# Kernel tuning notes

Measured on AMD Instinct MI355X. Metric: run time of the kernel, lower is better.

The kernel has to match this reference:

```python
import jax, jax.numpy as jnp
import numpy as np
from jax import lax


def setup_inputs() -> dict:
    key = jax.random.key(0)
    k1, k2 = jax.random.split(key)
    B, H, W, Cin, Cout, kh, kw = 16, 128, 128, 128, 128, 3, 3
    X = jax.random.normal(k1, (B, H, W, Cin), dtype=jnp.float32)
    kernel = jax.random.normal(k2, (B, kh, kw, Cin, Cout), dtype=jnp.float32) * 0.05
    return {"X": X, "kernel": kernel}


def _conv_one(x, k):
    # x: [H, W, Cin]; k: [kh, kw, Cin, Cout] -> [H', W', Cout]
    out = lax.conv_general_dilated(
        x[None],  # [1, H, W, Cin]
        k,
        window_strides=(1, 1),
        padding='VALID',
        dimension_numbers=('NHWC', 'HWIO', 'NHWC'),
    )
    return out[0]


def reference(X, kernel):
    # Per-sample dynamic-filter conv: each batch element convolved with its own
    # [kh, kw, Cin, Cout] filter. Equivalent to the TF depthwise-reshape trick
    # followed by reduce_sum over the input-channel axis.
    return jax.vmap(_conv_one)(X, kernel)  # [B, H', W', Cout]
```

## Files before the change

### kernel.cpp

```cpp
#include <hip/hip_runtime.h>
#include <cstdint>

#define OWD 126
#define MTOT 15876

typedef short bf16x8 __attribute__((ext_vector_type(8)));
typedef float f32x4  __attribute__((ext_vector_type(4)));

#define BT_ELEMS  (16u * 128u * 1152u)
#define XBF_ELEMS (16u * 128u * 128u * 128u)
#define WS_NEEDED ((size_t)(BT_ELEMS + XBF_ELEMS) * 2)

__device__ __forceinline__ uint16_t f2bf(float f) {
    union { float f; uint32_t u; } v;
    v.f = f;
    uint32_t u = v.u;
    return (uint16_t)((u + 0x7FFFu + ((u >> 16) & 1u)) >> 16);
}

__device__ __forceinline__ uint32_t pk2(float a, float b) {
    return (uint32_t)f2bf(a) | ((uint32_t)f2bf(b) << 16);
}

__device__ __forceinline__ void gl_lds16(const uint16_t* g, uint16_t* l) {
    __builtin_amdgcn_global_load_lds(
        (const __attribute__((address_space(1))) uint32_t*)g,
        (__attribute__((address_space(3))) uint32_t*)l, 16, 0, 0);
}

__global__ __launch_bounds__(256) void kprep(const float* __restrict__ Kin,
                                             uint16_t* __restrict__ Bt) {
    const int rs = blockIdx.x;
    const int b  = blockIdx.y;
    const int t  = threadIdx.x;
    const int n  = t & 127;
    const int og = t >> 7;

    const float* src = Kin + (((size_t)b * 9 + rs) << 14);
    uint16_t*    dst = Bt + ((size_t)b * 128 + n) * 1152 + rs * 128;

#pragma unroll
    for (int o = 0; o < 8; ++o) {
        const int oct = og * 8 + o;
        const float* s0 = src + (oct * 8) * 128 + n;
        uint4 p;
        p.x = pk2(s0[0 * 128], s0[1 * 128]);
        p.y = pk2(s0[2 * 128], s0[3 * 128]);
        p.z = pk2(s0[4 * 128], s0[5 * 128]);
        p.w = pk2(s0[6 * 128], s0[7 * 128]);
        *(uint4*)(dst + oct * 8) = p;
    }
}

__global__ __launch_bounds__(256) void xprep(const float* __restrict__ X,
                                             uint16_t* __restrict__ Xbf) {
    const size_t i = ((size_t)blockIdx.x * 256 + threadIdx.x) * 8;
    const float4 a = *(const float4*)(X + i);
    const float4 b = *(const float4*)(X + i + 4);
    uint4 p;
    p.x = pk2(a.x, a.y);
    p.y = pk2(a.z, a.w);
    p.z = pk2(b.x, b.y);
    p.w = pk2(b.z, b.w);
    *(uint4*)(Xbf + i) = p;
}

__global__ __launch_bounds__(256) void conv_mfma_c(const uint16_t* __restrict__ Xbf,
                                                   const uint16_t* __restrict__ Bt,
                                                   float* __restrict__ Out) {
    __shared__ __align__(16) uint16_t lds[3][256 * 32];

    const int id    = blockIdx.x + 125 * blockIdx.y;
    const int nid   = (id & 7) * 250 + (id >> 3);
    const int mtile = nid % 125;
    const int b     = nid / 125;

    const int tid  = threadIdx.x;
    const int lane = tid & 63;
    const int wave = tid >> 6;
    const int wm   = (wave & 1) << 6;
    const int wn   = (wave >> 1) << 6;
    const int l15  = lane & 15;
    const int quad = lane >> 4;

    const int l2 = lane >> 2;
    const int kc = (lane & 3) ^ ((lane >> 3) & 3);
    const uint16_t* Asrc[2];
    const uint16_t* Bsrc[2];
#pragma unroll
    for (int i = 0; i < 2; ++i) {
        const int row = wave * 32 + i * 16 + l2;
        int m = mtile * 128 + row;
        if (m >= MTOT) m = MTOT - 1;
        const int oh = m / OWD, ow = m - oh * OWD;
        Asrc[i] = Xbf + (((size_t)b * 128 + oh) * 128 + ow) * 128 + kc * 8;
        Bsrc[i] = Bt + ((size_t)b * 128 + row) * 1152 + kc * 8;
    }
    const int dbase = wave * 1024 + lane * 8;

    f32x4 acc[4][4];
#pragma unroll
    for (int i = 0; i < 4; ++i)
#pragma unroll
        for (int j = 0; j < 4; ++j)
            acc[i][j] = (f32x4){0.f, 0.f, 0.f, 0.f};

#define STAGE(t_, bu_)                                                      \
    {                                                                       \
        const int rs_ = (t_) >> 2;                                         \
        const int c0_ = ((t_) & 3) << 5;                                   \
        const int r_  = (rs_ * 11) >> 5;                \
        const int s_  = rs_ - r_ * 3;                                      \
        const int ao_ = (r_ * 128 + s_) * 128 + c0_;                       \
        const int bo_ = rs_ * 128 + c0_;                                   \
        uint16_t* Ad_ = &lds[bu_][dbase];                                  \
        uint16_t* Bd_ = &lds[bu_][4096 + dbase];                           \
        _Pragma("unroll")                                                  \
        for (int i_ = 0; i_ < 2; ++i_) {                                   \
            gl_lds16(Asrc[i_] + ao_, Ad_ + i_ * 512);                      \
            gl_lds16(Bsrc[i_] + bo_, Bd_ + i_ * 512);                      \
        }                                                                  \
    }

#define COMPUTE(bu_)                                                        \
    {                                                                       \
        bf16x8 af[4], bfr[4];                                              \
        _Pragma("unroll")                                                  \
        for (int i_ = 0; i_ < 4; ++i_) {                                   \
            const int row_ = wm + i_ * 16 + l15;                           \
            const int sl_  = quad ^ ((row_ >> 1) & 3);                     \
            af[i_] = *(const bf16x8*)&lds[bu_][row_ * 32 + sl_ * 8];       \
        }                                                                  \
        _Pragma("unroll")                                                  \
        for (int j_ = 0; j_ < 4; ++j_) {                                   \
            const int row_ = wn + j_ * 16 + l15;                           \
            const int sl_  = quad ^ ((row_ >> 1) & 3);                     \
            bfr[j_] = *(const bf16x8*)&lds[bu_][4096 + row_ * 32 + sl_ * 8];\
        }                                                                  \
        __builtin_amdgcn_s_setprio(1);                                     \
        _Pragma("unroll")                                                  \
        for (int i_ = 0; i_ < 4; ++i_)                                     \
            _Pragma("unroll")                                              \
            for (int j_ = 0; j_ < 4; ++j_)                                 \
                acc[i_][j_] = __builtin_amdgcn_mfma_f32_16x16x32_bf16(     \
                    af[i_], bfr[j_], acc[i_][j_], 0, 0, 0);                \
        __builtin_amdgcn_s_setprio(0);                                     \
    }

#define WAITBAR4                                                            \
    asm volatile("s_waitcnt vmcnt(4)" ::: "memory");                       \
    __builtin_amdgcn_s_barrier();                                          \
    __builtin_amdgcn_sched_barrier(0);

#define ITER(t_, bc_, bs_)                                                  \
    {                                                                       \
        WAITBAR4;                                                          \
        STAGE((t_) + 2, bs_);                                              \
        COMPUTE(bc_);                                                      \
    }

    STAGE(0, 0);
    STAGE(1, 1);

#pragma unroll 1
    for (int t = 0; t < 33; t += 3) {
        ITER(t, 0, 2);
        ITER(t + 1, 1, 0);
        ITER(t + 2, 2, 1);
    }
    ITER(33, 0, 2);
    WAITBAR4;
    COMPUTE(1);
    asm volatile("s_waitcnt vmcnt(0)" ::: "memory");
    __builtin_amdgcn_s_barrier();
    __builtin_amdgcn_sched_barrier(0);
    COMPUTE(2);

#undef STAGE
#undef COMPUTE
#undef WAITBAR4
#undef ITER

#pragma unroll
    for (int i = 0; i < 4; ++i) {
#pragma unroll
        for (int rr = 0; rr < 4; ++rr) {
            const int mrow = mtile * 128 + wm + i * 16 + quad * 4 + rr;
            if (mrow < MTOT) {
                const int oh2 = mrow / OWD;
                const int ow2 = mrow - oh2 * OWD;
                float* op = Out + (((size_t)b * OWD + oh2) * OWD + ow2) * 128 + wn + l15;
#pragma unroll
                for (int j = 0; j < 4; ++j)
                    op[j * 16] = acc[i][j][rr];
            }
        }
    }
}

__global__ __launch_bounds__(256) void conv_mfma(const float* __restrict__ X,
                                                 const uint16_t* __restrict__ Bt,
                                                 float* __restrict__ Out) {
    __shared__ __align__(16) uint16_t lA[128 * 64];
    __shared__ __align__(16) uint16_t lB[128 * 64];

    const int mtile = blockIdx.x;
    const int b     = blockIdx.y;
    const int tid   = threadIdx.x;
    const int lane  = tid & 63;
    const int wave  = tid >> 6;
    const int wm    = (wave & 1) << 6;
    const int wn    = (wave >> 1) << 6;
    const int l15   = lane & 15;
    const int quad  = lane >> 4;

    const int srow  = tid >> 1;
    const int shalf = tid & 1;

    int m = mtile * 128 + srow;
    if (m >= MTOT) m = MTOT - 1;
    const int oh = m / OWD;
    const int ow = m - oh * OWD;
    const float*    Xb = X + (((size_t)b * 128 + oh) * 128 + ow) * 128;
    const uint16_t* Bb = Bt + ((size_t)b * 128 + srow) * 1152 + shalf * 32;

    f32x4 acc[4][4];
#pragma unroll
    for (int i = 0; i < 4; ++i)
#pragma unroll
        for (int j = 0; j < 4; ++j)
            acc[i][j] = (f32x4){0.f, 0.f, 0.f, 0.f};

    for (int chunk = 0; chunk < 18; ++chunk) {
        const int rs = chunk >> 1;
        const int c0 = (chunk & 1) << 6;
        const int r  = rs / 3;
        const int s  = rs - r * 3;

        __syncthreads();
        {
            const float4* src = (const float4*)(Xb + (r * 128 + s) * 128 + c0 + shalf * 32);
            float4 v[8];
#pragma unroll
            for (int i = 0; i < 8; ++i) v[i] = src[i];
#pragma unroll
            for (int i = 0; i < 4; ++i) {
                uint4 p;
                p.x = pk2(v[2 * i].x, v[2 * i].y);
                p.y = pk2(v[2 * i].z, v[2 * i].w);
                p.z = pk2(v[2 * i + 1].x, v[2 * i + 1].y);
                p.w = pk2(v[2 * i + 1].z, v[2 * i + 1].w);
                const int ci = (shalf * 4 + i) ^ (srow & 7);
                *(uint4*)&lA[srow * 64 + ci * 8] = p;
            }
        }
        {
            const uint4* bsrc = (const uint4*)(Bb + rs * 128 + c0);
#pragma unroll
            for (int i = 0; i < 4; ++i) {
                const uint4 p = bsrc[i];
                const int ci = (shalf * 4 + i) ^ (srow & 7);
                *(uint4*)&lB[srow * 64 + ci * 8] = p;
            }
        }
        __syncthreads();

#pragma unroll
        for (int ksub = 0; ksub < 2; ++ksub) {
            bf16x8 af[4], bfr[4];
#pragma unroll
            for (int i = 0; i < 4; ++i) {
                const int row = wm + i * 16 + l15;
                const int ci  = (ksub * 4 + quad) ^ (row & 7);
                af[i] = *(const bf16x8*)&lA[row * 64 + ci * 8];
            }
#pragma unroll
            for (int j = 0; j < 4; ++j) {
                const int row = wn + j * 16 + l15;
                const int ci  = (ksub * 4 + quad) ^ (row & 7);
                bfr[j] = *(const bf16x8*)&lB[row * 64 + ci * 8];
            }
#pragma unroll
            for (int i = 0; i < 4; ++i)
#pragma unroll
                for (int j = 0; j < 4; ++j)
                    acc[i][j] = __builtin_amdgcn_mfma_f32_16x16x32_bf16(
                        af[i], bfr[j], acc[i][j], 0, 0, 0);
        }
    }

#pragma unroll
    for (int i = 0; i < 4; ++i) {
#pragma unroll
        for (int rr = 0; rr < 4; ++rr) {
            const int mrow = mtile * 128 + wm + i * 16 + quad * 4 + rr;
            if (mrow < MTOT) {
                const int oh2 = mrow / OWD;
                const int ow2 = mrow - oh2 * OWD;
                float* op = Out + (((size_t)b * OWD + oh2) * OWD + ow2) * 128 + wn + l15;
#pragma unroll
                for (int j = 0; j < 4; ++j)
                    op[j * 16] = acc[i][j][rr];
            }
        }
    }
}

extern "C" void kernel_launch(void* const* d_in, const int* in_sizes, int n_in,
                              void* d_out, int out_size, void* d_ws, size_t ws_size,
                              hipStream_t stream) {
    const float* X   = (const float*)d_in[0];
    const float* Kin = (const float*)d_in[1];
    float*       Out = (float*)d_out;
    uint16_t*    Bt  = (uint16_t*)d_ws;
    uint16_t*    Xbf = Bt + BT_ELEMS;

    kprep<<<dim3(9, 16), 256, 0, stream>>>(Kin, Bt);
    if (ws_size >= WS_NEEDED) {
        xprep<<<XBF_ELEMS / (256 * 8), 256, 0, stream>>>(X, Xbf);
        conv_mfma_c<<<dim3(125, 16), 256, 0, stream>>>(Xbf, Bt, Out);
    } else {
        conv_mfma<<<dim3(125, 16), 256, 0, stream>>>(X, Bt, Out);
    }
}
```

Baseline: 319.0 us.

## Enlarge conv GEMM tile to 256x128 with 8 waves and 64-wide K steps

Replaces the 128x128 tile, 4-wave kernel with a 256x128 tile using 512 threads (8 waves), each still computing a 64x64 subtile. The K step per stage doubles from 32 to 64 elements, halving the number of pipeline iterations and barriers, and the LDS swizzle is changed to suit 64-element rows. Each B tile is now reused across twice as many output rows, cutting global B traffic and staging overhead. The cost is larger LDS buffers (three stages of 48 KB each, about 144 KB), which may limit occupancy, plus a coarser grid of 1008 blocks.

```diff
diff --git a/kernel.cpp b/kernel.cpp
--- a/kernel.cpp
+++ b/kernel.cpp
@@ -65,38 +65,41 @@
     *(uint4*)(Xbf + i) = p;
 }
 
-__global__ __launch_bounds__(256) void conv_mfma_c(const uint16_t* __restrict__ Xbf,
-                                                   const uint16_t* __restrict__ Bt,
-                                                   float* __restrict__ Out) {
-    __shared__ __align__(16) uint16_t lds[3][256 * 32];
-
-    const int id    = blockIdx.x + 125 * blockIdx.y;
-    const int nid   = (id & 7) * 250 + (id >> 3);
-    const int mtile = nid % 125;
-    const int b     = nid / 125;
+__global__ __launch_bounds__(512, 2) void conv_mfma_e(const uint16_t* __restrict__ Xbf,
+                                                      const uint16_t* __restrict__ Bt,
+                                                      float* __restrict__ Out) {
+    __shared__ __align__(16) uint16_t lds[3][24576];
+
+    const int id    = blockIdx.x + 63 * blockIdx.y;
+    const int nid   = (id & 7) * 126 + (id >> 3);
+    const int mtile = nid % 63;
+    const int b     = nid / 63;
 
     const int tid  = threadIdx.x;
     const int lane = tid & 63;
     const int wave = tid >> 6;
-    const int wm   = (wave & 1) << 6;
-    const int wn   = (wave >> 1) << 6;
+    const int wm   = (wave & 3) << 6;
+    const int wn   = (wave >> 2) << 6;
     const int l15  = lane & 15;
     const int quad = lane >> 4;
 
-    const int l2 = lane >> 2;
-    const int kc = (lane & 3) ^ ((lane >> 3) & 3);
-    const uint16_t* Asrc[2];
+    const int kc = (lane & 7) ^ (lane >> 3);
+    const uint16_t* Asrc[4];
     const uint16_t* Bsrc[2];
 #pragma unroll
-    for (int i = 0; i < 2; ++i) {
-        const int row = wave * 32 + i * 16 + l2;
-        int m = mtile * 128 + row;
+    for (int p = 0; p < 4; ++p) {
+        const int row = p * 64 + wave * 8 + (lane >> 3);
+        int m = mtile * 256 + row;
         if (m >= MTOT) m = MTOT - 1;
         const int oh = m / OWD, ow = m - oh * OWD;
-        Asrc[i] = Xbf + (((size_t)b * 128 + oh) * 128 + ow) * 128 + kc * 8;
-        Bsrc[i] = Bt + ((size_t)b * 128 + row) * 1152 + kc * 8;
-    }
-    const int dbase = wave * 1024 + lane * 8;
+        Asrc[p] = Xbf + (((size_t)b * 128 + oh) * 128 + ow) * 128 + kc * 8;
+    }
+#pragma unroll
+    for (int q = 0; q < 2; ++q) {
+        const int row = q * 64 + wave * 8 + (lane >> 3);
+        Bsrc[q] = Bt + ((size_t)b * 128 + row) * 1152 + kc * 8;
+    }
+    const int dbase = tid * 8;
 
     f32x4 acc[4][4];
 #pragma unroll
@@ -107,54 +110,59 @@
 
 #define STAGE(t_, bu_)                                                      \
     {                                                                       \
-        const int rs_ = (t_) >> 2;                                         \
-        const int c0_ = ((t_) & 3) << 5;                                   \
+        const int rs_ = (t_) >> 1;                                         \
+        const int c0_ = ((t_) & 1) << 6;                                   \
         const int r_  = (rs_ * 11) >> 5;                \
         const int s_  = rs_ - r_ * 3;                                      \
         const int ao_ = (r_ * 128 + s_) * 128 + c0_;                       \
         const int bo_ = rs_ * 128 + c0_;                                   \
-        uint16_t* Ad_ = &lds[bu_][dbase];                                  \
-        uint16_t* Bd_ = &lds[bu_][4096 + dbase];                           \
+        uint16_t* base_ = &lds[bu_][0];                                    \
         _Pragma("unroll")                                                  \
-        for (int i_ = 0; i_ < 2; ++i_) {                                   \
-            gl_lds16(Asrc[i_] + ao_, Ad_ + i_ * 512);                      \
-            gl_lds16(Bsrc[i_] + bo_, Bd_ + i_ * 512);                      \
-        }                                                                  \
+        for (int p_ = 0; p_ < 4; ++p_)                                     \
+            gl_lds16(Asrc[p_] + ao_, base_ + p_ * 4096 + dbase);           \
+        _Pragma("unroll")                                                  \
+        for (int q_ = 0; q_ < 2; ++q_)                                     \
+            gl_lds16(Bsrc[q_] + bo_, base_ + 16384 + q_ * 4096 + dbase);   \
     }
 
 #define COMPUTE(bu_)                                                        \
     {                                                                       \
-        bf16x8 af[4], bfr[4];                                              \
+        bf16x8 af[2][4], bfr[2][4];                                        \
         _Pragma("unroll")                                                  \
-        for (int i_ = 0; i_ < 4; ++i_) {                                   \
-            const int row_ = wm + i_ * 16 + l15;                           \
-            const int sl_  = quad ^ ((row_ >> 1) & 3);                     \
-            af[i_] = *(const bf16x8*)&lds[bu_][row_ * 32 + sl_ * 8];       \
-        }                                                                  \
-        _Pragma("unroll")                                                  \
-        for (int j_ = 0; j_ < 4; ++j_) {                                   \
-            const int row_ = wn + j_ * 16 + l15;                           \
-            const int sl_  = quad ^ ((row_ >> 1) & 3);                     \
-            bfr[j_] = *(const bf16x8*)&lds[bu_][4096 + row_ * 32 + sl_ * 8];\
+        for (int h_ = 0; h_ < 2; ++h_) {                                   \
+            _Pragma("unroll")                                              \
+            for (int i_ = 0; i_ < 4; ++i_) {                               \
+                const int row_ = wm + i_ * 16 + l15;                       \
+                const int sl_  = (h_ * 4 + quad) ^ (row_ & 7);             \
+                af[h_][i_] = *(const bf16x8*)&lds[bu_][row_ * 64 + sl_ * 8];\
+            }                                                              \
+            _Pragma("unroll")                                              \
+            for (int j_ = 0; j_ < 4; ++j_) {                               \
+                const int row_ = wn + j_ * 16 + l15;                       \
+                const int sl_  = (h_ * 4 + quad) ^ (row_ & 7);             \
+                bfr[h_][j_] = *(const bf16x8*)&lds[bu_][16384 + row_ * 64 + sl_ * 8];\
+            }                                                              \
         }                                                                  \
         __builtin_amdgcn_s_setprio(1);                                     \
         _Pragma("unroll")                                                  \
-        for (int i_ = 0; i_ < 4; ++i_)                                     \
+        for (int h_ = 0; h_ < 2; ++h_)                                     \
             _Pragma("unroll")                                              \
-            for (int j_ = 0; j_ < 4; ++j_)                                 \
-                acc[i_][j_] = __builtin_amdgcn_mfma_f32_16x16x32_bf16(     \
-                    af[i_], bfr[j_], acc[i_][j_], 0, 0, 0);                \
+            for (int i_ = 0; i_ < 4; ++i_)                                 \
+                _Pragma("unroll")                                          \
+                for (int j_ = 0; j_ < 4; ++j_)                             \
+                    acc[i_][j_] = __builtin_amdgcn_mfma_f32_16x16x32_bf16( \
+                        af[h_][i_], bfr[h_][j_], acc[i_][j_], 0, 0, 0);    \
         __builtin_amdgcn_s_setprio(0);                                     \
     }
 
-#define WAITBAR4                                                            \
-    asm volatile("s_waitcnt vmcnt(4)" ::: "memory");                       \
+#define WAITBAR(n_)                                                         \
+    asm volatile("s_waitcnt vmcnt(" #n_ ")" ::: "memory");                 \
     __builtin_amdgcn_s_barrier();                                          \
     __builtin_amdgcn_sched_barrier(0);
 
 #define ITER(t_, bc_, bs_)                                                  \
     {                                                                       \
-        WAITBAR4;                                                          \
+        WAITBAR(6);                                                        \
         STAGE((t_) + 2, bs_);                                              \
         COMPUTE(bc_);                                                      \
     }
@@ -163,29 +171,27 @@
     STAGE(1, 1);
 
 #pragma unroll 1
-    for (int t = 0; t < 33; t += 3) {
+    for (int t = 0; t < 15; t += 3) {
         ITER(t, 0, 2);
         ITER(t + 1, 1, 0);
         ITER(t + 2, 2, 1);
     }
-    ITER(33, 0, 2);
-    WAITBAR4;
+    ITER(15, 0, 2);
+    WAITBAR(6);
     COMPUTE(1);
-    asm volatile("s_waitcnt vmcnt(0)" ::: "memory");
-    __builtin_amdgcn_s_barrier();
-    __builtin_amdgcn_sched_barrier(0);
+    WAITBAR(0);
     COMPUTE(2);
 
 #undef STAGE
 #undef COMPUTE
-#undef WAITBAR4
+#undef WAITBAR
 #undef ITER
 
 #pragma unroll
     for (int i = 0; i < 4; ++i) {
 #pragma unroll
         for (int rr = 0; rr < 4; ++rr) {
-            const int mrow = mtile * 128 + wm + i * 16 + quad * 4 + rr;
+            const int mrow = mtile * 256 + wm + i * 16 + quad * 4 + rr;
             if (mrow < MTOT) {
                 const int oh2 = mrow / OWD;
                 const int ow2 = mrow - oh2 * OWD;
@@ -318,7 +324,7 @@
     kprep<<<dim3(9, 16), 256, 0, stream>>>(Kin, Bt);
     if (ws_size >= WS_NEEDED) {
         xprep<<<XBF_ELEMS / (256 * 8), 256, 0, stream>>>(X, Xbf);
-        conv_mfma_c<<<dim3(125, 16), 256, 0, stream>>>(Xbf, Bt, Out);
+        conv_mfma_e<<<dim3(63, 16), 512, 0, stream>>>(Xbf, Bt, Out);
     } else {
         conv_mfma<<<dim3(125, 16), 256, 0, stream>>>(X, Bt, Out);
     }
```

Result: no change. 316.5 us (-0.8%).

## Enlarge conv GEMM block tile to 256x128 with 8 waves

Applied to the files above, without the earlier changes.

The block tile grows from 128x128 to 256x128 output rows, using 512 threads (8 waves) per block. The grid halves to 63x16 blocks. Each 128-row B (filter) tile is now loaded once per 256 output rows instead of per 128, cutting B global traffic and LDS staging per output. The cost is 72KB of LDS per block across the triple buffer, fewer blocks to fill the CUs (1008 blocks), and padding waste in the last M tile.

```diff
diff --git a/kernel.cpp b/kernel.cpp
--- a/kernel.cpp
+++ b/kernel.cpp
@@ -65,38 +65,38 @@
     *(uint4*)(Xbf + i) = p;
 }
 
-__global__ __launch_bounds__(256) void conv_mfma_c(const uint16_t* __restrict__ Xbf,
-                                                   const uint16_t* __restrict__ Bt,
-                                                   float* __restrict__ Out) {
-    __shared__ __align__(16) uint16_t lds[3][256 * 32];
-
-    const int id    = blockIdx.x + 125 * blockIdx.y;
-    const int nid   = (id & 7) * 250 + (id >> 3);
-    const int mtile = nid % 125;
-    const int b     = nid / 125;
+__global__ __launch_bounds__(512, 4) void conv_mfma_f(const uint16_t* __restrict__ Xbf,
+                                                      const uint16_t* __restrict__ Bt,
+                                                      float* __restrict__ Out) {
+    __shared__ __align__(16) uint16_t lds[3][12288];
+
+    const int id    = blockIdx.x + 63 * blockIdx.y;
+    const int nid   = (id & 7) * 126 + (id >> 3);
+    const int mtile = nid % 63;
+    const int b     = nid / 63;
 
     const int tid  = threadIdx.x;
     const int lane = tid & 63;
     const int wave = tid >> 6;
-    const int wm   = (wave & 1) << 6;
-    const int wn   = (wave >> 1) << 6;
+    const int wm   = (wave & 3) << 6;
+    const int wn   = (wave >> 2) << 6;
     const int l15  = lane & 15;
     const int quad = lane >> 4;
 
-    const int l2 = lane >> 2;
-    const int kc = (lane & 3) ^ ((lane >> 3) & 3);
+    const int srow = tid >> 2;
+    const int kc   = (tid & 3) ^ ((tid >> 3) & 3);
     const uint16_t* Asrc[2];
-    const uint16_t* Bsrc[2];
-#pragma unroll
-    for (int i = 0; i < 2; ++i) {
-        const int row = wave * 32 + i * 16 + l2;
-        int m = mtile * 128 + row;
+    const uint16_t* Bsrc1;
+#pragma unroll
+    for (int p = 0; p < 2; ++p) {
+        const int row = p * 128 + srow;
+        int m = mtile * 256 + row;
         if (m >= MTOT) m = MTOT - 1;
         const int oh = m / OWD, ow = m - oh * OWD;
-        Asrc[i] = Xbf + (((size_t)b * 128 + oh) * 128 + ow) * 128 + kc * 8;
-        Bsrc[i] = Bt + ((size_t)b * 128 + row) * 1152 + kc * 8;
-    }
-    const int dbase = wave * 1024 + lane * 8;
+        Asrc[p] = Xbf + (((size_t)b * 128 + oh) * 128 + ow) * 128 + kc * 8;
+    }
+    Bsrc1 = Bt + ((size_t)b * 128 + srow) * 1152 + kc * 8;
+    const int dbase = tid * 8;
 
     f32x4 acc[4][4];
 #pragma unroll
@@ -113,13 +113,11 @@
         const int s_  = rs_ - r_ * 3;                                      \
         const int ao_ = (r_ * 128 + s_) * 128 + c0_;                       \
         const int bo_ = rs_ * 128 + c0_;                                   \
-        uint16_t* Ad_ = &lds[bu_][dbase];                                  \
-        uint16_t* Bd_ = &lds[bu_][4096 + dbase];                           \
+        uint16_t* base_ = &lds[bu_][0];                                    \
         _Pragma("unroll")                                                  \
-        for (int i_ = 0; i_ < 2; ++i_) {                                   \
-            gl_lds16(Asrc[i_] + ao_, Ad_ + i_ * 512);                      \
-            gl_lds16(Bsrc[i_] + bo_, Bd_ + i_ * 512);                      \
-        }                                                                  \
+        for (int p_ = 0; p_ < 2; ++p_)                                     \
+            gl_lds16(Asrc[p_] + ao_, base_ + p_ * 4096 + dbase);           \
+        gl_lds16(Bsrc1 + bo_, base_ + 8192 + dbase);                       \
     }
 
 #define COMPUTE(bu_)                                                        \
@@ -135,7 +133,7 @@
         for (int j_ = 0; j_ < 4; ++j_) {                                   \
             const int row_ = wn + j_ * 16 + l15;                           \
             const int sl_  = quad ^ ((row_ >> 1) & 3);                     \
-            bfr[j_] = *(const bf16x8*)&lds[bu_][4096 + row_ * 32 + sl_ * 8];\
+            bfr[j_] = *(const bf16x8*)&lds[bu_][8192 + row_ * 32 + sl_ * 8];\
         }                                                                  \
         __builtin_amdgcn_s_setprio(1);                                     \
         _Pragma("unroll")                                                  \
@@ -147,14 +145,14 @@
         __builtin_amdgcn_s_setprio(0);                                     \
     }
 
-#define WAITBAR4                                                            \
-    asm volatile("s_waitcnt vmcnt(4)" ::: "memory");                       \
+#define WAITBAR(n_)                                                         \
+    asm volatile("s_waitcnt vmcnt(" #n_ ")" ::: "memory");                 \
     __builtin_amdgcn_s_barrier();                                          \
     __builtin_amdgcn_sched_barrier(0);
 
 #define ITER(t_, bc_, bs_)                                                  \
     {                                                                       \
-        WAITBAR4;                                                          \
+        WAITBAR(3);                                                        \
         STAGE((t_) + 2, bs_);                                              \
         COMPUTE(bc_);                                                      \
     }
@@ -169,23 +167,21 @@
         ITER(t + 2, 2, 1);
     }
     ITER(33, 0, 2);
-    WAITBAR4;
+    WAITBAR(3);
     COMPUTE(1);
-    asm volatile("s_waitcnt vmcnt(0)" ::: "memory");
-    __builtin_amdgcn_s_barrier();
-    __builtin_amdgcn_sched_barrier(0);
+    WAITBAR(0);
     COMPUTE(2);
 
 #undef STAGE
 #undef COMPUTE
-#undef WAITBAR4
+#undef WAITBAR
 #undef ITER
 
 #pragma unroll
     for (int i = 0; i < 4; ++i) {
 #pragma unroll
         for (int rr = 0; rr < 4; ++rr) {
-            const int mrow = mtile * 128 + wm + i * 16 + quad * 4 + rr;
+            const int mrow = mtile * 256 + wm + i * 16 + quad * 4 + rr;
             if (mrow < MTOT) {
                 const int oh2 = mrow / OWD;
                 const int ow2 = mrow - oh2 * OWD;
@@ -318,7 +314,7 @@
     kprep<<<dim3(9, 16), 256, 0, stream>>>(Kin, Bt);
     if (ws_size >= WS_NEEDED) {
         xprep<<<XBF_ELEMS / (256 * 8), 256, 0, stream>>>(X, Xbf);
-        conv_mfma_c<<<dim3(125, 16), 256, 0, stream>>>(Xbf, Bt, Out);
+        conv_mfma_f<<<dim3(63, 16), 512, 0, stream>>>(Xbf, Bt, Out);
     } else {
         conv_mfma<<<dim3(125, 16), 256, 0, stream>>>(X, Bt, Out);
     }
```

Result: no change. 315.2 us (-1.2%).
